# Kernel optimization log

Measured on AMD Instinct MI355X. Metric: run time of the kernel, lower is better.

The kernel has to match this reference:

```python
import jax, jax.numpy as jnp
import numpy as np

BETA = 0.2

def setup_inputs() -> dict:
    key = jax.random.key(0)
    k1, k2 = jax.random.split(key)
    z = jax.random.normal(k1, (32, 256, 32, 32), dtype=jnp.float32)
    # codebook initialized uniform(-1/K, 1/K) as in the torch module
    K, D = 8192, 256
    codebook = jax.random.uniform(k2, (K, D), dtype=jnp.float32, minval=-1.0 / K, maxval=1.0 / K)
    return {"z": z, "codebook": codebook}

def reference(z, codebook):
    b, d, h, w = z.shape
    # (b d h w) -> (b*h*w, d)
    zf = jnp.transpose(z, (0, 2, 3, 1)).reshape(-1, d)
    # squared L2 distances to codebook entries: [N, K]
    dist = (
        jnp.sum(zf * zf, axis=1, keepdims=True)
        + jnp.sum(codebook * codebook, axis=1)
        - 2.0 * jnp.matmul(zf, codebook.T)
    )
    indices = jnp.argmin(dist, axis=1)  # [N]
    # gather == one-hot matmul in value (and in gradient wrt codebook)
    quantized = jnp.take(codebook, indices, axis=0)  # [N, d]
    codebook_loss = jnp.mean((jax.lax.stop_gradient(zf) - quantized) ** 2)
    commitment_loss = BETA * jnp.mean((zf - jax.lax.stop_gradient(quantized)) ** 2)
    # straight-through estimator
    q_st = zf + jax.lax.stop_gradient(quantized - zf)
    q_st = jnp.transpose(q_st.reshape(b, h, w, d), (0, 3, 1, 2))
    return (q_st, codebook_loss, commitment_loss)
```

## Files before the change

kernel.cpp:

```cpp
#include <hip/hip_runtime.h>
#include <hip/hip_bf16.h>
#include <stdint.h>

typedef __attribute__((ext_vector_type(4))) float floatx4;
typedef __attribute__((ext_vector_type(16))) float floatx16;
typedef __attribute__((ext_vector_type(4))) int intx4;
typedef __attribute__((ext_vector_type(8))) int intx8;
typedef __attribute__((ext_vector_type(2))) unsigned int uint2v;
typedef unsigned long long u64;

typedef __attribute__((address_space(1))) const uint32_t ga_u32;
typedef __attribute__((address_space(3))) uint32_t ls_u32;

static constexpr int NROWS = 32768;
static constexpr int NCODE = 8192;
static constexpr int QELEMS = 8388608;
static constexpr float CSCALE = 8192.0f;

__global__ __launch_bounds__(256) void prep_all(
    const float* __restrict__ z, const float* __restrict__ cb,
    unsigned char* __restrict__ z8, unsigned char* __restrict__ c8,
    float* __restrict__ norms, u64* __restrict__ amin)
{
  const int bid = blockIdx.x;
  const int t = threadIdx.x;
  if (bid < 1024) {
    __shared__ float tile[32][260];
    const int b = bid & 31, db = (bid >> 5) & 7, hwb = bid >> 8;
    const int d0 = db * 32, hw0 = hwb * 256;
    const float* src = z + (((size_t)b * 256 + d0) << 10) + hw0;
#pragma unroll
    for (int i = 0; i < 8; ++i) {
      int idx = i * 256 + t;
      int r = idx >> 6, c4 = (idx & 63) * 4;
      *(floatx4*)&tile[r][c4] = *(const floatx4*)&src[((size_t)r << 10) + c4];
    }
    __syncthreads();
    const int dq = t & 3;
    const int hb = t >> 2;
#pragma unroll
    for (int it = 0; it < 4; ++it) {
      int h = hb + it * 64;
      float f[8];
#pragma unroll
      for (int i = 0; i < 8; ++i) f[i] = tile[dq * 8 + i][h];
      int lo = __builtin_amdgcn_cvt_pk_fp8_f32(f[0], f[1], 0, false);
      lo = __builtin_amdgcn_cvt_pk_fp8_f32(f[2], f[3], lo, true);
      int hi = __builtin_amdgcn_cvt_pk_fp8_f32(f[4], f[5], 0, false);
      hi = __builtin_amdgcn_cvt_pk_fp8_f32(f[6], f[7], hi, true);
      uint2v o; o[0] = (unsigned)lo; o[1] = (unsigned)hi;
      *(uint2v*)&z8[((size_t)(b * 1024 + hw0 + h)) * 256 + d0 + dq * 8] = o;
    }
  } else if (bid < 3072) {
    const int k = (bid - 1024) * 4 + (t >> 6);
    const int lane = t & 63;
    floatx4 v = *(const floatx4*)&cb[((size_t)k << 8) + lane * 4];
    float a = v[0] * CSCALE, b2 = v[1] * CSCALE, c = v[2] * CSCALE, d2 = v[3] * CSCALE;
    int r = __builtin_amdgcn_cvt_pk_fp8_f32(a, b2, 0, false);
    r = __builtin_amdgcn_cvt_pk_fp8_f32(c, d2, r, true);
    *(unsigned int*)&c8[((size_t)k << 8) + lane * 4] = (unsigned)r;
    float s = a * a + b2 * b2 + c * c + d2 * d2;
#pragma unroll
    for (int off = 32; off; off >>= 1) s += __shfl_down(s, off);
    if (lane == 0) norms[k] = s;
  } else {
    const int base = (bid - 3072) * 2048;
#pragma unroll
    for (int i = 0; i < 8; ++i) amin[base + i * 256 + t] = ~0ull;
  }
}

__global__ __launch_bounds__(256, 2) void gemm_argmin(
    const unsigned char* __restrict__ z8, const unsigned char* __restrict__ c8,
    const float* __restrict__ norms, u64* __restrict__ amin)
{
  __shared__ alignas(16) unsigned char lds8[65536 + 4096];

  const int tid = threadIdx.x;
  const int lane = tid & 63;
  const int wid = tid >> 6;
  const int wm = wid >> 1;
  const int wn = wid & 1;

  const int bid = blockIdx.x;
  const int swz = (bid & 7) * 1024 + (bid >> 3);
  const int cx = swz & 63;
  const int cy = swz >> 6;
  const int m0 = cx * 128;
  const int n0 = cy * 256;

  const int l31 = lane & 31;
  const int hi = lane >> 5;
  const int k2 = hi << 1;

  intx8 af[2][4];
#pragma unroll
  for (int ti = 0; ti < 2; ++ti) {
    const unsigned char* arow = c8 + ((size_t)(m0 + wm * 64 + ti * 32 + l31) << 8);
#pragma unroll
    for (int kt = 0; kt < 4; ++kt) {
      intx4 lo = *(const intx4*)(arow + kt * 64 + k2 * 16);
      intx4 hv = *(const intx4*)(arow + kt * 64 + k2 * 16 + 16);
      intx8 o;
#pragma unroll
      for (int w = 0; w < 4; ++w) { o[w] = lo[w]; o[4 + w] = hv[w]; }
      af[ti][kt] = o;
    }
  }

  floatx4 nv[2][4];
#pragma unroll
  for (int ti = 0; ti < 2; ++ti)
#pragma unroll
    for (int rq = 0; rq < 4; ++rq)
      nv[ti][rq] = *(const floatx4*)&norms[m0 + wm * 64 + ti * 32 + rq * 8 + 4 * hi];

#pragma unroll
  for (int p = 0; p < 16; ++p) {
    int f = p * 256 + tid;
    int row = f >> 4, sp = f & 15;
    int ls = sp ^ ((row >> 1) & 7);
    const unsigned char* gp = z8 + ((size_t)(n0 + row) << 8) + ls * 16;
    __builtin_amdgcn_global_load_lds((ga_u32*)gp, (ls_u32*)(lds8 + f * 16), 16, 0, 0);
  }
  asm volatile("s_waitcnt vmcnt(0)" ::: "memory");
  __builtin_amdgcn_s_barrier();
  asm volatile("" ::: "memory");

  floatx16 acc[2][4];
#pragma unroll
  for (int i = 0; i < 2; ++i)
#pragma unroll
    for (int j = 0; j < 4; ++j)
#pragma unroll
      for (int e = 0; e < 16; ++e) acc[i][j][e] = 0.f;

#pragma unroll
  for (int kt = 0; kt < 4; ++kt) {
    intx8 bf[4];
#pragma unroll
    for (int tj = 0; tj < 4; ++tj) {
      int row = wn * 128 + tj * 32 + l31;
      const unsigned char* rbase = lds8 + row * 256;
      int msk = (row >> 1) & 7;
      int L0 = kt * 4 + k2;
      intx4 lo = *(const intx4*)(rbase + ((L0 ^ msk) << 4));
      intx4 hv = *(const intx4*)(rbase + (((L0 + 1) ^ msk) << 4));
      intx8 o;
#pragma unroll
      for (int w = 0; w < 4; ++w) { o[w] = lo[w]; o[4 + w] = hv[w]; }
      bf[tj] = o;
    }
#pragma unroll
    for (int ti = 0; ti < 2; ++ti)
#pragma unroll
      for (int tj = 0; tj < 4; ++tj)
        acc[ti][tj] = __builtin_amdgcn_mfma_scale_f32_32x32x64_f8f6f4(
            af[ti][kt], bf[tj], acc[ti][tj], 0, 0, 0, 127, 0, 127);
  }

  u64* best2 = (u64*)(lds8 + 65536);
#pragma unroll
  for (int tj = 0; tj < 4; ++tj) {
    float best = __builtin_inff();
    int bc = 0;
#pragma unroll
    for (int ti = 0; ti < 2; ++ti)
#pragma unroll
      for (int rq = 0; rq < 4; ++rq)
#pragma unroll
        for (int rl = 0; rl < 4; ++rl) {
          float sc = fmaf(acc[ti][tj][rq * 4 + rl], -16384.f, nv[ti][rq][rl]);
          int cd = m0 + wm * 64 + ti * 32 + rq * 8 + 4 * hi + rl;
          if (sc < best) { best = sc; bc = cd; }
        }
    uint32_t u = __float_as_uint(best);
    u ^= ((uint32_t)((int32_t)u >> 31) | 0x80000000u);
    u64 p = ((u64)u << 32) | (uint32_t)bc;
    {
      u64 o = (u64)__shfl_xor((long long)p, 32);
      p = o < p ? o : p;
    }
    if (lane < 32) best2[(size_t)(wn * 128 + tj * 32 + l31) * 2 + wm] = p;
  }
  __syncthreads();
  {
    u64 a = best2[tid * 2], b = best2[tid * 2 + 1];
    u64 p = a < b ? a : b;
    atomicMin(&amin[n0 + tid], p);
  }
}

__global__ __launch_bounds__(256) void gather_out(
    const float* __restrict__ z, const float* __restrict__ cb,
    const u64* __restrict__ amin,
    float* __restrict__ out, float* __restrict__ partial)
{
  const int t = threadIdx.x;
  const size_t e0 = ((size_t)blockIdx.x * 256 + t) * 8;
  const int d = (int)((e0 >> 10) & 255);
  const int b = (int)(e0 >> 18);
  const int n0 = b * 1024 + (int)(e0 & 1023);
  uint32_t kv[8];
#pragma unroll
  for (int m = 0; m < 8; ++m) kv[m] = (uint32_t)amin[n0 + m];
  floatx4 z0 = *(const floatx4*)&z[e0];
  floatx4 z1 = *(const floatx4*)&z[e0 + 4];
  floatx4 q0, q1;
#pragma unroll
  for (int m = 0; m < 4; ++m) {
    q0[m] = cb[((size_t)kv[m] << 8) + d];
    q1[m] = cb[((size_t)kv[4 + m] << 8) + d];
  }
  *(floatx4*)&out[e0] = q0;
  *(floatx4*)&out[e0 + 4] = q1;
  float s = 0.f;
#pragma unroll
  for (int m = 0; m < 4; ++m) {
    float d0 = z0[m] - q0[m], d1 = z1[m] - q1[m];
    s += d0 * d0 + d1 * d1;
  }
#pragma unroll
  for (int off = 32; off; off >>= 1) s += __shfl_down(s, off);
  __shared__ float ps[4];
  if ((t & 63) == 0) ps[t >> 6] = s;
  __syncthreads();
  if (t == 0) partial[blockIdx.x] = ps[0] + ps[1] + ps[2] + ps[3];
}

__global__ __launch_bounds__(256) void finalize(const float* __restrict__ partial,
                                                float* __restrict__ out)
{
  const int t = threadIdx.x;
  float s = 0.f;
#pragma unroll
  for (int i = 0; i < 16; ++i) s += partial[i * 256 + t];
#pragma unroll
  for (int off = 32; off; off >>= 1) s += __shfl_down(s, off);
  __shared__ float ps[4];
  if ((t & 63) == 0) ps[t >> 6] = s;
  __syncthreads();
  if (t == 0) {
    float m = (ps[0] + ps[1] + ps[2] + ps[3]) / (float)QELEMS;
    out[QELEMS] = m;
    out[QELEMS + 1] = 0.2f * m;
  }
}

extern "C" void kernel_launch(void* const* d_in, const int* in_sizes, int n_in,
                              void* d_out, int out_size, void* d_ws, size_t ws_size,
                              hipStream_t stream)
{
  const float* z = (const float*)d_in[0];
  const float* cb = (const float*)d_in[1];
  float* out = (float*)d_out;
  char* ws = (char*)d_ws;

  unsigned char* z8 = (unsigned char*)(ws + 0);
  unsigned char* c8 = (unsigned char*)(ws + 8388608);
  float* norms = (float*)(ws + 10485760);
  u64* amin = (u64*)(ws + 10616832);
  float* lpart = (float*)(ws + 10878976);

  prep_all<<<3088, 256, 0, stream>>>(z, cb, z8, c8, norms, amin);
  gemm_argmin<<<8192, 256, 0, stream>>>(z8, c8, norms, amin);
  gather_out<<<QELEMS / 2048, 256, 0, stream>>>(z, cb, amin, out, lpart);
  finalize<<<1, 256, 0, stream>>>(lpart, out);
}
```

Measured before the change: 173.3 us.

## Pre-swizzle fp8 operands into MFMA fragment layout and drop LDS staging

The prep kernel now writes both the fp8 codebook and the fp8 latents in a fragment-ordered layout, so each lane's MFMA operand is a contiguous 16-byte global load. The GEMM kernel no longer stages the latent tile through LDS. Each block loops over four 256-row latent tiles while keeping its codebook fragments in registers, which cuts the grid from 8192 to 2048 blocks. The per-block LDS reduction is replaced by direct per-wave atomicMin. This removes LDS traffic and barriers and amortizes codebook loads, at the cost of more global atomics and no cross-wave sharing of latent loads.

```diff
diff --git a/kernel.cpp b/kernel.cpp
--- a/kernel.cpp
+++ b/kernel.cpp
@@ -9,17 +9,15 @@
 typedef __attribute__((ext_vector_type(2))) unsigned int uint2v;
 typedef unsigned long long u64;
 
-typedef __attribute__((address_space(1))) const uint32_t ga_u32;
-typedef __attribute__((address_space(3))) uint32_t ls_u32;
-
 static constexpr int NROWS = 32768;
 static constexpr int NCODE = 8192;
 static constexpr int QELEMS = 8388608;
 static constexpr float CSCALE = 8192.0f;
 
+
 __global__ __launch_bounds__(256) void prep_all(
     const float* __restrict__ z, const float* __restrict__ cb,
-    unsigned char* __restrict__ z8, unsigned char* __restrict__ c8,
+    unsigned char* __restrict__ z8f, unsigned char* __restrict__ c8f,
     float* __restrict__ norms, u64* __restrict__ amin)
 {
   const int bid = blockIdx.x;
@@ -49,7 +47,10 @@
       int hi = __builtin_amdgcn_cvt_pk_fp8_f32(f[4], f[5], 0, false);
       hi = __builtin_amdgcn_cvt_pk_fp8_f32(f[6], f[7], hi, true);
       uint2v o; o[0] = (unsigned)lo; o[1] = (unsigned)hi;
-      *(uint2v*)&z8[((size_t)(b * 1024 + hw0 + h)) * 256 + d0 + dq * 8] = o;
+      int t32 = b * 32 + hwb * 8 + (h >> 5);
+      int slot = db * 2 + (dq >> 1);
+      size_t addr = (size_t)t32 * 8192 + slot * 512 + (h & 31) * 16 + (dq & 1) * 8;
+      *(uint2v*)&z8f[addr] = o;
     }
   } else if (bid < 3072) {
     const int k = (bid - 1024) * 4 + (t >> 6);
@@ -58,7 +59,8 @@
     float a = v[0] * CSCALE, b2 = v[1] * CSCALE, c = v[2] * CSCALE, d2 = v[3] * CSCALE;
     int r = __builtin_amdgcn_cvt_pk_fp8_f32(a, b2, 0, false);
     r = __builtin_amdgcn_cvt_pk_fp8_f32(c, d2, r, true);
-    *(unsigned int*)&c8[((size_t)k << 8) + lane * 4] = (unsigned)r;
+    size_t addr = (size_t)(k >> 5) * 8192 + (lane >> 2) * 512 + (k & 31) * 16 + (lane & 3) * 4;
+    *(unsigned int*)&c8f[addr] = (unsigned)r;
     float s = a * a + b2 * b2 + c * c + d2 * d2;
 #pragma unroll
     for (int off = 32; off; off >>= 1) s += __shfl_down(s, off);
@@ -71,11 +73,9 @@
 }
 
 __global__ __launch_bounds__(256, 2) void gemm_argmin(
-    const unsigned char* __restrict__ z8, const unsigned char* __restrict__ c8,
+    const unsigned char* __restrict__ z8f, const unsigned char* __restrict__ c8f,
     const float* __restrict__ norms, u64* __restrict__ amin)
 {
-  __shared__ alignas(16) unsigned char lds8[65536 + 4096];
-
   const int tid = threadIdx.x;
   const int lane = tid & 63;
   const int wid = tid >> 6;
@@ -83,11 +83,10 @@
   const int wn = wid & 1;
 
   const int bid = blockIdx.x;
-  const int swz = (bid & 7) * 1024 + (bid >> 3);
+  const int swz = (bid & 7) * 256 + (bid >> 3);
   const int cx = swz & 63;
-  const int cy = swz >> 6;
+  const int cyg = swz >> 6;
   const int m0 = cx * 128;
-  const int n0 = cy * 256;
 
   const int l31 = lane & 31;
   const int hi = lane >> 5;
@@ -96,11 +95,12 @@
   intx8 af[2][4];
 #pragma unroll
   for (int ti = 0; ti < 2; ++ti) {
-    const unsigned char* arow = c8 + ((size_t)(m0 + wm * 64 + ti * 32 + l31) << 8);
+    const unsigned char* ab = c8f + (size_t)((m0 >> 5) + wm * 2 + ti) * 8192
+                              + (size_t)k2 * 512 + l31 * 16;
 #pragma unroll
     for (int kt = 0; kt < 4; ++kt) {
-      intx4 lo = *(const intx4*)(arow + kt * 64 + k2 * 16);
-      intx4 hv = *(const intx4*)(arow + kt * 64 + k2 * 16 + 16);
+      intx4 lo = *(const intx4*)(ab + kt * 2048);
+      intx4 hv = *(const intx4*)(ab + kt * 2048 + 512);
       intx8 o;
 #pragma unroll
       for (int w = 0; w < 4; ++w) { o[w] = lo[w]; o[4 + w] = hv[w]; }
@@ -115,79 +115,64 @@
     for (int rq = 0; rq < 4; ++rq)
       nv[ti][rq] = *(const floatx4*)&norms[m0 + wm * 64 + ti * 32 + rq * 8 + 4 * hi];
 
-#pragma unroll
-  for (int p = 0; p < 16; ++p) {
-    int f = p * 256 + tid;
-    int row = f >> 4, sp = f & 15;
-    int ls = sp ^ ((row >> 1) & 7);
-    const unsigned char* gp = z8 + ((size_t)(n0 + row) << 8) + ls * 16;
-    __builtin_amdgcn_global_load_lds((ga_u32*)gp, (ls_u32*)(lds8 + f * 16), 16, 0, 0);
-  }
-  asm volatile("s_waitcnt vmcnt(0)" ::: "memory");
-  __builtin_amdgcn_s_barrier();
-  asm volatile("" ::: "memory");
-
-  floatx16 acc[2][4];
-#pragma unroll
-  for (int i = 0; i < 2; ++i)
-#pragma unroll
-    for (int j = 0; j < 4; ++j)
-#pragma unroll
-      for (int e = 0; e < 16; ++e) acc[i][j][e] = 0.f;
-
-#pragma unroll
-  for (int kt = 0; kt < 4; ++kt) {
-    intx8 bf[4];
+  const unsigned char* bb = z8f + (size_t)(cyg * 32 + wn * 4) * 8192
+                            + (size_t)k2 * 512 + (size_t)l31 * 16;
+
+#pragma unroll 1
+  for (int t = 0; t < 4; ++t) {
+    floatx16 acc[2][4];
+#pragma unroll
+    for (int i = 0; i < 2; ++i)
+#pragma unroll
+      for (int j = 0; j < 4; ++j)
+#pragma unroll
+        for (int e = 0; e < 16; ++e) acc[i][j][e] = 0.f;
+
+    const unsigned char* tb = bb + (size_t)t * 65536;
+#pragma unroll
+    for (int kt = 0; kt < 4; ++kt) {
+      intx8 bf[4];
+#pragma unroll
+      for (int tj = 0; tj < 4; ++tj) {
+        intx4 lo = *(const intx4*)(tb + tj * 8192 + kt * 2048);
+        intx4 hv = *(const intx4*)(tb + tj * 8192 + kt * 2048 + 512);
+        intx8 o;
+#pragma unroll
+        for (int w = 0; w < 4; ++w) { o[w] = lo[w]; o[4 + w] = hv[w]; }
+        bf[tj] = o;
+      }
+#pragma unroll
+      for (int ti = 0; ti < 2; ++ti)
+#pragma unroll
+        for (int tj = 0; tj < 4; ++tj)
+          acc[ti][tj] = __builtin_amdgcn_mfma_scale_f32_32x32x64_f8f6f4(
+              af[ti][kt], bf[tj], acc[ti][tj], 0, 0, 0, 127, 0, 127);
+    }
+
 #pragma unroll
     for (int tj = 0; tj < 4; ++tj) {
-      int row = wn * 128 + tj * 32 + l31;
-      const unsigned char* rbase = lds8 + row * 256;
-      int msk = (row >> 1) & 7;
-      int L0 = kt * 4 + k2;
-      intx4 lo = *(const intx4*)(rbase + ((L0 ^ msk) << 4));
-      intx4 hv = *(const intx4*)(rbase + (((L0 + 1) ^ msk) << 4));
-      intx8 o;
-#pragma unroll
-      for (int w = 0; w < 4; ++w) { o[w] = lo[w]; o[4 + w] = hv[w]; }
-      bf[tj] = o;
-    }
-#pragma unroll
-    for (int ti = 0; ti < 2; ++ti)
-#pragma unroll
-      for (int tj = 0; tj < 4; ++tj)
-        acc[ti][tj] = __builtin_amdgcn_mfma_scale_f32_32x32x64_f8f6f4(
-            af[ti][kt], bf[tj], acc[ti][tj], 0, 0, 0, 127, 0, 127);
-  }
-
-  u64* best2 = (u64*)(lds8 + 65536);
-#pragma unroll
-  for (int tj = 0; tj < 4; ++tj) {
-    float best = __builtin_inff();
-    int bc = 0;
-#pragma unroll
-    for (int ti = 0; ti < 2; ++ti)
-#pragma unroll
-      for (int rq = 0; rq < 4; ++rq)
-#pragma unroll
-        for (int rl = 0; rl < 4; ++rl) {
-          float sc = fmaf(acc[ti][tj][rq * 4 + rl], -16384.f, nv[ti][rq][rl]);
-          int cd = m0 + wm * 64 + ti * 32 + rq * 8 + 4 * hi + rl;
-          if (sc < best) { best = sc; bc = cd; }
-        }
-    uint32_t u = __float_as_uint(best);
-    u ^= ((uint32_t)((int32_t)u >> 31) | 0x80000000u);
-    u64 p = ((u64)u << 32) | (uint32_t)bc;
-    {
-      u64 o = (u64)__shfl_xor((long long)p, 32);
-      p = o < p ? o : p;
-    }
-    if (lane < 32) best2[(size_t)(wn * 128 + tj * 32 + l31) * 2 + wm] = p;
-  }
-  __syncthreads();
-  {
-    u64 a = best2[tid * 2], b = best2[tid * 2 + 1];
-    u64 p = a < b ? a : b;
-    atomicMin(&amin[n0 + tid], p);
+      float best = __builtin_inff();
+      int bc = 0;
+#pragma unroll
+      for (int ti = 0; ti < 2; ++ti)
+#pragma unroll
+        for (int rq = 0; rq < 4; ++rq)
+#pragma unroll
+          for (int rl = 0; rl < 4; ++rl) {
+            float sc = fmaf(acc[ti][tj][rq * 4 + rl], -16384.f, nv[ti][rq][rl]);
+            int cd = m0 + wm * 64 + ti * 32 + rq * 8 + 4 * hi + rl;
+            if (sc < best) { best = sc; bc = cd; }
+          }
+      uint32_t u = __float_as_uint(best);
+      u ^= ((uint32_t)((int32_t)u >> 31) | 0x80000000u);
+      u64 p = ((u64)u << 32) | (uint32_t)bc;
+      {
+        u64 o = (u64)__shfl_xor((long long)p, 32);
+        p = o < p ? o : p;
+      }
+      if (lane < 32)
+        atomicMin(&amin[cyg * 1024 + t * 256 + wn * 128 + tj * 32 + l31], p);
+    }
   }
 }
 
@@ -256,14 +241,14 @@
   float* out = (float*)d_out;
   char* ws = (char*)d_ws;
 
-  unsigned char* z8 = (unsigned char*)(ws + 0);
-  unsigned char* c8 = (unsigned char*)(ws + 8388608);
+  unsigned char* z8f = (unsigned char*)(ws + 0);
+  unsigned char* c8f = (unsigned char*)(ws + 8388608);
   float* norms = (float*)(ws + 10485760);
   u64* amin = (u64*)(ws + 10616832);
   float* lpart = (float*)(ws + 10878976);
 
-  prep_all<<<3088, 256, 0, stream>>>(z, cb, z8, c8, norms, amin);
-  gemm_argmin<<<8192, 256, 0, stream>>>(z8, c8, norms, amin);
+  prep_all<<<3088, 256, 0, stream>>>(z, cb, z8f, c8f, norms, amin);
+  gemm_argmin<<<2048, 256, 0, stream>>>(z8f, c8f, norms, amin);
   gather_out<<<QELEMS / 2048, 256, 0, stream>>>(z, cb, amin, out, lpart);
   finalize<<<1, 256, 0, stream>>>(lpart, out);
 }
```

New measurement: 188.5 us. +8.7%, slower.
